# Kernel optimization log

Hardware: AMD Instinct MI355X
Metric: run time of the kernel (lower is better)

## Reference

```python
import math
import jax, jax.numpy as jnp
import numpy as np

N_HEADS = 16  # matches init_kwargs n_heads

def setup_inputs() -> dict:
    key = jax.random.key(0)
    ks = jax.random.split(key, 6)
    B, T, D = 1, 2048, 1024
    x = jax.random.normal(ks[0], (B, T, D), dtype=jnp.float32)
    # binary causal mask, broadcast over batch: [B, T, T]
    mask = jnp.broadcast_to(jnp.tril(jnp.ones((T, T), dtype=jnp.float32)), (B, T, T))
    shift = jax.random.uniform(ks[1], (B, T, T), dtype=jnp.float32)
    W = jax.random.normal(ks[2], (D, 3 * D), dtype=jnp.float32) * (1.0 / math.sqrt(D))
    b = jnp.zeros((3 * D,), dtype=jnp.float32)
    Wo = jax.random.normal(ks[3], (D, D), dtype=jnp.float32) * (1.0 / math.sqrt(D))
    bo = jnp.zeros((D,), dtype=jnp.float32)
    return {"x": x, "mask": mask, "shift": shift, "W": W, "b": b, "Wo": Wo, "bo": bo}

def reference(x, mask, shift, W, b, Wo, bo):
    B, T, D = x.shape
    H = N_HEADS
    dh = D // H
    qkv = x @ W + b  # [B,T,3D]
    # torch: chunk(H) -> stack -> chunk(3): head h uses block [h*3*dh : (h+1)*3*dh],
    # split as (q, k, v) of size dh each => reshape last dim to (H, 3, dh)
    qkv = qkv.reshape(B, T, H, 3, dh)
    q = jnp.moveaxis(qkv[..., 0, :], 2, 0)  # [H,B,T,dh]
    k = jnp.moveaxis(qkv[..., 1, :], 2, 0)
    v = jnp.moveaxis(qkv[..., 2, :], 2, 0)
    logits = jnp.einsum('hbqd,hbkd->hbqk', q, k) / math.sqrt(dh)  # [H,B,T,T]
    logits = logits * mask - 1e6 * (1.0 - mask)  # mask [B,T,T] broadcasts over H
    # per-head ALiBi-like scale: exp(-log(2) * h / 2)
    scale = jnp.exp(-math.log(2.0) * jnp.arange(H, dtype=jnp.float32) / 2.0)
    logits = logits - scale.reshape(H, 1, 1, 1) * shift
    att = jax.nn.softmax(logits, axis=-1)
    o = jnp.einsum('hbqk,hbkd->hbqd', att, v)  # [H,B,T,dh]
    o = jnp.moveaxis(o, 0, 2).reshape(B, T, D)  # concat heads on last dim
    o = o @ Wo + bo
    k_out = jnp.moveaxis(k, 0, 2).reshape(B, T, D)
    v_out = jnp.moveaxis(v, 0, 2).reshape(B, T, D)
    return (o, k_out, v_out)
```

## Files before the change

kernel.cpp:

```cpp
#include <hip/hip_runtime.h>
#include <hip/hip_bf16.h>

typedef __attribute__((ext_vector_type(8))) short bfrag8;
typedef __attribute__((ext_vector_type(4))) short short4v;
typedef __attribute__((ext_vector_type(4))) float f32x4;
typedef __attribute__((ext_vector_type(8))) unsigned short ushort8;
typedef __attribute__((ext_vector_type(4))) unsigned short ushort4v;

__device__ __forceinline__ float bf2f(unsigned short u) {
  unsigned int v = ((unsigned int)u) << 16;
  return __builtin_bit_cast(float, v);
}
__device__ __forceinline__ unsigned short f2bf(float f) {
  unsigned int u = __builtin_bit_cast(unsigned int, f);
  u += 0x7fffu + ((u >> 16) & 1u);
  return (unsigned short)(u >> 16);
}

#define GLDS(gp, lp) __builtin_amdgcn_global_load_lds( \
    (__attribute__((address_space(1))) void*)(gp), \
    (__attribute__((address_space(3))) void*)(lp), 16, 0, 0)

__device__ __forceinline__ bool inputs_are_f32(const unsigned int* mw) {
  return mw[0] == 0x3F800000u;
}

__global__ __launch_bounds__(256) void prep_kernel(
    const void* __restrict__ x, const void* __restrict__ b,
    const void* __restrict__ bo, const void* __restrict__ W,
    const void* __restrict__ Wo,
    unsigned short* __restrict__ xc, unsigned short* __restrict__ bc,
    unsigned short* __restrict__ boc, unsigned short* __restrict__ Wt,
    unsigned short* __restrict__ Wot,
    const unsigned int* __restrict__ mw) {
  const bool isf32 = inputs_are_f32(mw);
  const int bid = blockIdx.x, tid = threadIdx.x;
  __shared__ unsigned short tile[64][72];

  if (bid < 2052) {
    const void* src; unsigned short* dst; int base, n4;
    if (bid < 2048)      { src = x;  dst = xc;  base = bid;        n4 = 2048 * 1024 / 4; }
    else if (bid < 2051) { src = b;  dst = bc;  base = bid - 2048; n4 = 3072 / 4; }
    else                 { src = bo; dst = boc; base = 0;          n4 = 1024 / 4; }
    int i = base * 256 + tid;
    if (i >= n4) return;
    ushort4v o;
    if (isf32) {
      const float* s = (const float*)src;
      o[0] = f2bf(s[i * 4 + 0]); o[1] = f2bf(s[i * 4 + 1]);
      o[2] = f2bf(s[i * 4 + 2]); o[3] = f2bf(s[i * 4 + 3]);
    } else {
      o = *(const ushort4v*)((const unsigned short*)src + (size_t)i * 4);
    }
    *(ushort4v*)(dst + (size_t)i * 4) = o;
    return;
  }

  const void* src; unsigned short* dst; int R, C, bx, by;
  if (bid < 2820) { src = W;  dst = Wt;  R = 1024; C = 3072;
                    int e = bid - 2052; bx = e % 48; by = e / 48; }
  else            { src = Wo; dst = Wot; R = 1024; C = 1024;
                    int e = bid - 2820; bx = e % 16; by = e / 16; }
  const int r0 = by << 6, c0 = bx << 6;
  #pragma unroll
  for (int i = 0; i < 16; ++i) {
    int e = i * 256 + tid;
    int r = e >> 6, c = e & 63;
    size_t idx = (size_t)(r0 + r) * C + c0 + c;
    tile[r][c] = isf32 ? f2bf(((const float*)src)[idx])
                       : ((const unsigned short*)src)[idx];
  }
  __syncthreads();
  #pragma unroll
  for (int i = 0; i < 16; ++i) {
    int e = i * 256 + tid;
    int c = e >> 6, r = e & 63;
    dst[(size_t)(c0 + c) * R + r0 + r] = tile[r][c];
  }
}

template <int BN, int EPI>
__global__ __launch_bounds__(256) void gemm_bt(
    const unsigned short* __restrict__ A,
    const unsigned short* __restrict__ Bt,
    const unsigned short* __restrict__ bias,
    unsigned short* __restrict__ Cbf,
    float* __restrict__ kout,
    float* __restrict__ vout,
    float* __restrict__ Cf,
    int M, int N, int K) {
  constexpr int NT = BN / 32;
  __shared__ __align__(16) unsigned short As[128 * 32];
  __shared__ __align__(16) unsigned short Bs[BN * 32];
  const int tid = threadIdx.x;
  const int wave = tid >> 6, lane = tid & 63;
  const int q8 = lane >> 4, l15 = lane & 15;
  const int m0 = blockIdx.y << 7, n0 = blockIdx.x * BN;
  const int wm = (wave >> 1) << 6, wn = (wave & 1) * (BN / 2);

  f32x4 acc[4][NT];
  #pragma unroll
  for (int i = 0; i < 4; ++i)
    #pragma unroll
    for (int t = 0; t < NT; ++t) acc[i][t] = (f32x4){0.f, 0.f, 0.f, 0.f};

  const int cidb = wave * 64 + lane;
  for (int k0 = 0; k0 < K; k0 += 32) {
    __syncthreads();
    #pragma unroll
    for (int j = 0; j < 2; ++j) {
      int cid = j * 256 + cidb;
      int row = cid >> 2, co = (cid & 3) << 3;
      GLDS(A + (size_t)(m0 + row) * K + k0 + co, As + (size_t)(j * 256 + wave * 64) * 8);
    }
    #pragma unroll
    for (int j = 0; j < BN / 64; ++j) {
      int cid = j * 256 + cidb;
      int row = cid >> 2, co = (cid & 3) << 3;
      GLDS(Bt + (size_t)(n0 + row) * K + k0 + co, Bs + (size_t)(j * 256 + wave * 64) * 8);
    }
    __builtin_amdgcn_s_waitcnt(0);
    __syncthreads();
    bfrag8 af[4], bfr[NT];
    #pragma unroll
    for (int i = 0; i < 4; ++i)
      af[i] = *(const bfrag8*)(As + (wm + i * 16 + l15) * 32 + q8 * 8);
    #pragma unroll
    for (int t = 0; t < NT; ++t)
      bfr[t] = *(const bfrag8*)(Bs + (wn + t * 16 + l15) * 32 + q8 * 8);
    #pragma unroll
    for (int i = 0; i < 4; ++i)
      #pragma unroll
      for (int t = 0; t < NT; ++t)
        acc[i][t] = __builtin_amdgcn_mfma_f32_16x16x32_bf16(af[i], bfr[t], acc[i][t], 0, 0, 0);
  }

  #pragma unroll
  for (int t = 0; t < NT; ++t) {
    const int col = n0 + wn + t * 16 + l15;
    const float bv = bf2f(bias[col]);
    #pragma unroll
    for (int i = 0; i < 4; ++i) {
      #pragma unroll
      for (int r = 0; r < 4; ++r) {
        const int row = m0 + wm + i * 16 + q8 * 4 + r;
        const float fv = acc[i][t][r] + bv;
        if (EPI) {
          Cbf[(size_t)row * N + col] = f2bf(fv);
          int h = col / 192, rr = col - h * 192;
          if (rr >= 128)      vout[(size_t)row * 1024 + h * 64 + (rr - 128)] = fv;
          else if (rr >= 64)  kout[(size_t)row * 1024 + h * 64 + (rr - 64)] = fv;
        } else {
          Cf[(size_t)row * N + col] = fv;
        }
      }
    }
  }
}

__global__ __launch_bounds__(256) void attn_kernel(
    const unsigned short* __restrict__ qkv,
    const void* __restrict__ shift,
    unsigned short* __restrict__ Pon,
    float* __restrict__ Mst,
    float* __restrict__ Lst,
    const unsigned int* __restrict__ mw) {
  const bool isf32 = inputs_are_f32(mw);
  __shared__ __align__(16) unsigned short Qs[64 * 64];
  __shared__ __align__(16) unsigned short Ks[64 * 64];
  __shared__ __align__(16) unsigned short VTs[64 * 64];
  __shared__ __align__(16) short Ps[4 * 16 * 64];

  const int tid = threadIdx.x;
  const int wave = tid >> 6, lane = tid & 63;
  const int q8 = lane >> 4, l15 = lane & 15;
  const int bid = blockIdx.x;
  const int qb = 31 - (bid >> 5);
  const int h = bid & 15, part = (bid >> 4) & 1;
  const int q0 = qb << 6;
  const int count = qb + 1, c0 = (count + 1) >> 1;
  const int kbeg = part ? c0 : 0;
  const int kend = part ? count : c0;
  const float scale_h = exp2f(-0.5f * (float)h);
  const float NEG = -1e30f;

  #pragma unroll
  for (int j = 0; j < 2; ++j) {
    int cid = j * 256 + wave * 64 + lane;
    int row = cid >> 3, ci = cid & 7;
    ushort8 qv = *(const ushort8*)(qkv + (size_t)(q0 + row) * 3072 + h * 192 + ci * 8);
    *(ushort8*)(Qs + row * 64 + ((ci ^ (row & 7)) << 3)) = qv;
  }

  const int cidA = wave * 64 + lane;
  const int rowA = cidA >> 3, ciA = cidA & 7;
  const int cidB = 256 + cidA;
  const int rowB = cidB >> 3, ciB = cidB & 7;

  float mrow = NEG, lrow = 0.f;
  f32x4 oacc[4];
  #pragma unroll
  for (int t = 0; t < 4; ++t) oacc[t] = (f32x4){0.f, 0.f, 0.f, 0.f};
  const int qg = q0 + wave * 16 + l15;

  ushort8 kpfA, kpfB, vpf0, vpf1;
  float shf_nxt[4][4], shf_cur[4][4];

  {
    const int k0 = kbeg << 6;
    kpfA = *(const ushort8*)(qkv + (size_t)(k0 + rowA) * 3072 + h * 192 + 64 + ciA * 8);
    kpfB = *(const ushort8*)(qkv + (size_t)(k0 + rowB) * 3072 + h * 192 + 64 + ciB * 8);
    const unsigned short* vsrc = qkv + (size_t)(k0 + lane) * 3072 + h * 192 + 128 + wave * 16;
    vpf0 = *(const ushort8*)(vsrc);
    vpf1 = *(const ushort8*)(vsrc + 8);
    if (isf32) {
      const float* sp = (const float*)shift + (size_t)qg * 2048 + k0 + q8 * 4;
      #pragma unroll
      for (int mt = 0; mt < 4; ++mt) {
        f32x4 t4 = *(const f32x4*)(sp + mt * 16);
        shf_nxt[mt][0] = t4[0]; shf_nxt[mt][1] = t4[1];
        shf_nxt[mt][2] = t4[2]; shf_nxt[mt][3] = t4[3];
      }
    } else {
      const unsigned short* sp = (const unsigned short*)shift + (size_t)qg * 2048 + k0 + q8 * 4;
      #pragma unroll
      for (int mt = 0; mt < 4; ++mt) {
        ushort4v t4 = *(const ushort4v*)(sp + mt * 16);
        shf_nxt[mt][0] = bf2f(t4[0]); shf_nxt[mt][1] = bf2f(t4[1]);
        shf_nxt[mt][2] = bf2f(t4[2]); shf_nxt[mt][3] = bf2f(t4[3]);
      }
    }
  }

  for (int kt = kbeg; kt < kend; ++kt) {
    const int k0 = kt << 6;
    __syncthreads();
    *(ushort8*)(Ks + rowA * 64 + ((ciA ^ (rowA & 7)) << 3)) = kpfA;
    *(ushort8*)(Ks + rowB * 64 + ((ciB ^ (rowB & 7)) << 3)) = kpfB;
    #pragma unroll
    for (int j = 0; j < 8; ++j) {
      int d = wave * 16 + j;
      VTs[d * 64 + (((lane >> 3) ^ (d & 7)) << 3) + (lane & 7)] = vpf0[j];
      int d2 = d + 8;
      VTs[d2 * 64 + (((lane >> 3) ^ (d2 & 7)) << 3) + (lane & 7)] = vpf1[j];
    }
    #pragma unroll
    for (int mt = 0; mt < 4; ++mt)
      #pragma unroll
      for (int r = 0; r < 4; ++r) shf_cur[mt][r] = shf_nxt[mt][r];
    __syncthreads();

    if (kt + 1 < kend) {
      const int k0n = k0 + 64;
      kpfA = *(const ushort8*)(qkv + (size_t)(k0n + rowA) * 3072 + h * 192 + 64 + ciA * 8);
      kpfB = *(const ushort8*)(qkv + (size_t)(k0n + rowB) * 3072 + h * 192 + 64 + ciB * 8);
      const unsigned short* vsrc = qkv + (size_t)(k0n + lane) * 3072 + h * 192 + 128 + wave * 16;
      vpf0 = *(const ushort8*)(vsrc);
      vpf1 = *(const ushort8*)(vsrc + 8);
      if (isf32) {
        const float* sp = (const float*)shift + (size_t)qg * 2048 + k0n + q8 * 4;
        #pragma unroll
        for (int mt = 0; mt < 4; ++mt) {
          f32x4 t4 = *(const f32x4*)(sp + mt * 16);
          shf_nxt[mt][0] = t4[0]; shf_nxt[mt][1] = t4[1];
          shf_nxt[mt][2] = t4[2]; shf_nxt[mt][3] = t4[3];
        }
      } else {
        const unsigned short* sp = (const unsigned short*)shift + (size_t)qg * 2048 + k0n + q8 * 4;
        #pragma unroll
        for (int mt = 0; mt < 4; ++mt) {
          ushort4v t4 = *(const ushort4v*)(sp + mt * 16);
          shf_nxt[mt][0] = bf2f(t4[0]); shf_nxt[mt][1] = bf2f(t4[1]);
          shf_nxt[mt][2] = bf2f(t4[2]); shf_nxt[mt][3] = bf2f(t4[3]);
        }
      }
    }

    f32x4 st[4];
    #pragma unroll
    for (int mt = 0; mt < 4; ++mt) st[mt] = (f32x4){0.f, 0.f, 0.f, 0.f};
    #pragma unroll
    for (int kk = 0; kk < 2; ++kk) {
      int kc = kk * 4 + q8;
      int qrow = wave * 16 + l15;
      bfrag8 bq = *(const bfrag8*)(Qs + qrow * 64 + ((kc ^ (qrow & 7)) << 3));
      #pragma unroll
      for (int mt = 0; mt < 4; ++mt) {
        int krow = mt * 16 + l15;
        bfrag8 ak = *(const bfrag8*)(Ks + krow * 64 + ((kc ^ (krow & 7)) << 3));
        st[mt] = __builtin_amdgcn_mfma_f32_16x16x32_bf16(ak, bq, st[mt], 0, 0, 0);
      }
    }

    const bool diag = (kt == qb);
    float sv[4][4];
    float tmax = NEG;
    #pragma unroll
    for (int mt = 0; mt < 4; ++mt)
      #pragma unroll
      for (int r = 0; r < 4; ++r) {
        float s = st[mt][r] * 0.125f - scale_h * shf_cur[mt][r];
        if (diag) {
          int kg = k0 + mt * 16 + q8 * 4 + r;
          if (kg > qg) s = NEG;
        }
        sv[mt][r] = s;
        tmax = fmaxf(tmax, s);
      }
    tmax = fmaxf(tmax, __shfl_xor(tmax, 16, 64));
    tmax = fmaxf(tmax, __shfl_xor(tmax, 32, 64));
    const float mnew = fmaxf(mrow, tmax);
    const float alpha = __expf(mrow - mnew);
    float psum = 0.f;
    #pragma unroll
    for (int mt = 0; mt < 4; ++mt)
      #pragma unroll
      for (int r = 0; r < 4; ++r) {
        float p = __expf(sv[mt][r] - mnew);
        sv[mt][r] = p;
        psum += p;
      }
    psum += __shfl_xor(psum, 16, 64);
    psum += __shfl_xor(psum, 32, 64);
    lrow = lrow * alpha + psum;
    mrow = mnew;

    short* pw = Ps + wave * 1024;
    #pragma unroll
    for (int mt = 0; mt < 4; ++mt) {
      short4v pk;
      pk[0] = (short)f2bf(sv[mt][0]); pk[1] = (short)f2bf(sv[mt][1]);
      pk[2] = (short)f2bf(sv[mt][2]); pk[3] = (short)f2bf(sv[mt][3]);
      int kb = mt * 16 + q8 * 4;
      int chunk = (kb >> 3) ^ (l15 & 7);
      *(short4v*)(pw + l15 * 64 + (chunk << 3) + (kb & 7)) = pk;
    }

    float oal[4];
    #pragma unroll
    for (int r = 0; r < 4; ++r)
      oal[r] = __shfl(alpha, (lane & 48) | (q8 * 4 + r), 64);
    #pragma unroll
    for (int t = 0; t < 4; ++t)
      #pragma unroll
      for (int r = 0; r < 4; ++r) oacc[t][r] *= oal[r];

    __builtin_amdgcn_s_waitcnt(0xc07f);

    #pragma unroll
    for (int kk = 0; kk < 2; ++kk) {
      int kc = kk * 4 + q8;
      bfrag8 ap = *(const bfrag8*)(pw + l15 * 64 + ((kc ^ (l15 & 7)) << 3));
      #pragma unroll
      for (int t = 0; t < 4; ++t) {
        int drow = t * 16 + l15;
        bfrag8 bv = *(const bfrag8*)(VTs + drow * 64 + ((kc ^ (drow & 7)) << 3));
        oacc[t] = __builtin_amdgcn_mfma_f32_16x16x32_bf16(ap, bv, oacc[t], 0, 0, 0);
      }
    }
  }

  float linv[4];
  #pragma unroll
  for (int r = 0; r < 4; ++r) {
    float lr = __shfl(lrow, (lane & 48) | (q8 * 4 + r), 64);
    linv[r] = lr > 0.f ? 1.f / lr : 0.f;
  }
  const size_t pbase = ((size_t)(part * 16 + h) * 32 + qb) * 4096;
  #pragma unroll
  for (int t = 0; t < 4; ++t)
    #pragma unroll
    for (int r = 0; r < 4; ++r) {
      int rowl = wave * 16 + q8 * 4 + r;
      int coll = t * 16 + l15;
      Pon[pbase + rowl * 64 + coll] = f2bf(oacc[t][r] * linv[r]);
    }
  if (q8 == 0) {
    const size_t sbase = ((size_t)(part * 16 + h) * 32 + qb) * 64 + wave * 16 + l15;
    Mst[sbase] = mrow;
    Lst[sbase] = lrow;
  }
}

__global__ __launch_bounds__(256) void attn_merge(
    const unsigned short* __restrict__ Pon,
    const float* __restrict__ Mst, const float* __restrict__ Lst,
    unsigned short* __restrict__ oheads) {
  const int bid = blockIdx.x;
  const int h = bid >> 5, qb = bid & 31;
  const int t = threadIdx.x;
  const int q = t >> 2, dp = (t & 3) << 4;
  const size_t b0 = ((size_t)(0 * 16 + h) * 32 + qb);
  const size_t b1 = ((size_t)(1 * 16 + h) * 32 + qb);
  const float m0 = Mst[b0 * 64 + q], m1 = Mst[b1 * 64 + q];
  const float l0 = Lst[b0 * 64 + q], l1 = Lst[b1 * 64 + q];
  const float m = fmaxf(m0, m1);
  const float w0 = __expf(m0 - m) * l0, w1 = __expf(m1 - m) * l1;
  const float inv = 1.f / (w0 + w1);
  const unsigned short* p0 = Pon + b0 * 4096 + q * 64 + dp;
  const unsigned short* p1 = Pon + b1 * 4096 + q * 64 + dp;
  ushort8 a0 = *(const ushort8*)p0;
  ushort8 a1 = *(const ushort8*)(p0 + 8);
  ushort8 c0v = *(const ushort8*)p1;
  ushort8 c1v = *(const ushort8*)(p1 + 8);
  unsigned short* dst = oheads + (size_t)(qb * 64 + q) * 1024 + h * 64 + dp;
  ushort8 o0, o1;
  #pragma unroll
  for (int j = 0; j < 8; ++j) {
    o0[j] = f2bf((w0 * bf2f(a0[j]) + w1 * bf2f(c0v[j])) * inv);
    o1[j] = f2bf((w0 * bf2f(a1[j]) + w1 * bf2f(c1v[j])) * inv);
  }
  *(ushort8*)dst = o0;
  *(ushort8*)(dst + 8) = o1;
}

extern "C" void kernel_launch(void* const* d_in, const int* in_sizes, int n_in,
                              void* d_out, int out_size, void* d_ws, size_t ws_size,
                              hipStream_t stream) {
  const void* x     = d_in[0];
  const unsigned int* maskw = (const unsigned int*)d_in[1];
  const void* shift = d_in[2];
  const void* W     = d_in[3];
  const void* b     = d_in[4];
  const void* Wo    = d_in[5];
  const void* bo    = d_in[6];

  float* out   = (float*)d_out;
  float* o_out = out;
  float* k_out = out + (size_t)2048 * 1024;
  float* v_out = out + (size_t)2 * 2048 * 1024;

  unsigned short* ws     = (unsigned short*)d_ws;
  unsigned short* xc     = ws;
  unsigned short* bc     = xc + (size_t)2048 * 1024;
  unsigned short* boc    = bc + 3072;
  unsigned short* qkv    = boc + 1024;
  unsigned short* Wt     = qkv + (size_t)2048 * 3072;
  unsigned short* Wot    = Wt + (size_t)3072 * 1024;
  unsigned short* oheads = Wot + (size_t)1024 * 1024;
  unsigned short* Pon    = oheads + (size_t)2048 * 1024;
  float*          Mst    = (float*)(Pon + (size_t)2 * 16 * 32 * 4096);
  float*          Lst    = Mst + 65536;

  prep_kernel<<<3076, 256, 0, stream>>>(x, b, bo, W, Wo,
                                        xc, bc, boc, Wt, Wot, maskw);

  gemm_bt<128, 1><<<dim3(24, 16), 256, 0, stream>>>(
      xc, Wt, bc, qkv, k_out, v_out, nullptr, 2048, 3072, 1024);

  attn_kernel<<<1024, 256, 0, stream>>>(qkv, shift, Pon, Mst, Lst, maskw);

  attn_merge<<<512, 256, 0, stream>>>(Pon, Mst, Lst, oheads);

  gemm_bt<64, 0><<<dim3(16, 16), 256, 0, stream>>>(
      oheads, Wot, boc, nullptr, nullptr, nullptr, o_out, 2048, 1024, 1024);
}
```

Before: 202.7 us.

## Split attention into fixed 8-tile KV chunks with exp2 softmax and lazy rescale

Attention work is now split into KV chunks of at most 8 tiles per query block (up to 4 parts), replacing the two-way split, and the merge kernel combines up to four partials. The goal is better load balance across the causal triangle and more blocks. It also folds the softmax scale into log2 space so exp2 can be used, skips the output rescale when the running max grows by no more than 8, packs bf16 with a hardware convert instruction, raises MFMA wave priority, and adds an occupancy hint to the launch bounds. The lazy rescale lets unnormalised values grow by up to 2^8, which bf16 P can still represent, though it costs some precision. The extra partials add merge traffic.

```diff
diff --git a/kernel.cpp b/kernel.cpp
--- a/kernel.cpp
+++ b/kernel.cpp
@@ -6,6 +6,7 @@
 typedef __attribute__((ext_vector_type(4))) float f32x4;
 typedef __attribute__((ext_vector_type(8))) unsigned short ushort8;
 typedef __attribute__((ext_vector_type(4))) unsigned short ushort4v;
+typedef __attribute__((ext_vector_type(2))) unsigned int uint2v;
 
 __device__ __forceinline__ float bf2f(unsigned short u) {
   unsigned int v = ((unsigned int)u) << 16;
@@ -15,6 +16,11 @@
   unsigned int u = __builtin_bit_cast(unsigned int, f);
   u += 0x7fffu + ((u >> 16) & 1u);
   return (unsigned short)(u >> 16);
+}
+__device__ __forceinline__ unsigned int cvtpk_bf16(float a, float b) {
+  unsigned int r;
+  asm("v_cvt_pk_bf16_f32 %0, %1, %2" : "=v"(r) : "v"(a), "v"(b));
+  return r;
 }
 
 #define GLDS(gp, lp) __builtin_amdgcn_global_load_lds( \
@@ -158,7 +164,7 @@
   }
 }
 
-__global__ __launch_bounds__(256) void attn_kernel(
+__global__ __launch_bounds__(256, 5) void attn_kernel(
     const unsigned short* __restrict__ qkv,
     const void* __restrict__ shift,
     unsigned short* __restrict__ Pon,
@@ -175,13 +181,18 @@
   const int wave = tid >> 6, lane = tid & 63;
   const int q8 = lane >> 4, l15 = lane & 15;
   const int bid = blockIdx.x;
-  const int qb = 31 - (bid >> 5);
-  const int h = bid & 15, part = (bid >> 4) & 1;
+  const int h = bid & 15;
+  int pi = bid >> 4;
+  int qb = 31;
+  for (;;) { int npp = 1 + (qb >> 3); if (pi < npp) break; pi -= npp; --qb; }
+  const int part = pi;
   const int q0 = qb << 6;
-  const int count = qb + 1, c0 = (count + 1) >> 1;
-  const int kbeg = part ? c0 : 0;
-  const int kend = part ? count : c0;
-  const float scale_h = exp2f(-0.5f * (float)h);
+  const int count = qb + 1;
+  const int kbeg = part << 3;
+  const int kend = (kbeg + 8 < count) ? (kbeg + 8) : count;
+  const float LOG2E = 1.4426950408889634f;
+  const float c1 = 0.125f * LOG2E;
+  const float scale2 = __builtin_amdgcn_exp2f(-0.5f * (float)h) * LOG2E;
   const float NEG = -1e30f;
 
   #pragma unroll
@@ -218,16 +229,16 @@
       #pragma unroll
       for (int mt = 0; mt < 4; ++mt) {
         f32x4 t4 = *(const f32x4*)(sp + mt * 16);
-        shf_nxt[mt][0] = t4[0]; shf_nxt[mt][1] = t4[1];
-        shf_nxt[mt][2] = t4[2]; shf_nxt[mt][3] = t4[3];
+        shf_nxt[mt][0] = scale2 * t4[0]; shf_nxt[mt][1] = scale2 * t4[1];
+        shf_nxt[mt][2] = scale2 * t4[2]; shf_nxt[mt][3] = scale2 * t4[3];
       }
     } else {
       const unsigned short* sp = (const unsigned short*)shift + (size_t)qg * 2048 + k0 + q8 * 4;
       #pragma unroll
       for (int mt = 0; mt < 4; ++mt) {
         ushort4v t4 = *(const ushort4v*)(sp + mt * 16);
-        shf_nxt[mt][0] = bf2f(t4[0]); shf_nxt[mt][1] = bf2f(t4[1]);
-        shf_nxt[mt][2] = bf2f(t4[2]); shf_nxt[mt][3] = bf2f(t4[3]);
+        shf_nxt[mt][0] = scale2 * bf2f(t4[0]); shf_nxt[mt][1] = scale2 * bf2f(t4[1]);
+        shf_nxt[mt][2] = scale2 * bf2f(t4[2]); shf_nxt[mt][3] = scale2 * bf2f(t4[3]);
       }
     }
   }
@@ -262,16 +273,16 @@
         #pragma unroll
         for (int mt = 0; mt < 4; ++mt) {
           f32x4 t4 = *(const f32x4*)(sp + mt * 16);
-          shf_nxt[mt][0] = t4[0]; shf_nxt[mt][1] = t4[1];
-          shf_nxt[mt][2] = t4[2]; shf_nxt[mt][3] = t4[3];
+          shf_nxt[mt][0] = scale2 * t4[0]; shf_nxt[mt][1] = scale2 * t4[1];
+          shf_nxt[mt][2] = scale2 * t4[2]; shf_nxt[mt][3] = scale2 * t4[3];
         }
       } else {
         const unsigned short* sp = (const unsigned short*)shift + (size_t)qg * 2048 + k0n + q8 * 4;
         #pragma unroll
         for (int mt = 0; mt < 4; ++mt) {
           ushort4v t4 = *(const ushort4v*)(sp + mt * 16);
-          shf_nxt[mt][0] = bf2f(t4[0]); shf_nxt[mt][1] = bf2f(t4[1]);
-          shf_nxt[mt][2] = bf2f(t4[2]); shf_nxt[mt][3] = bf2f(t4[3]);
+          shf_nxt[mt][0] = scale2 * bf2f(t4[0]); shf_nxt[mt][1] = scale2 * bf2f(t4[1]);
+          shf_nxt[mt][2] = scale2 * bf2f(t4[2]); shf_nxt[mt][3] = scale2 * bf2f(t4[3]);
         }
       }
     }
@@ -279,6 +290,7 @@
     f32x4 st[4];
     #pragma unroll
     for (int mt = 0; mt < 4; ++mt) st[mt] = (f32x4){0.f, 0.f, 0.f, 0.f};
+    __builtin_amdgcn_s_setprio(1);
     #pragma unroll
     for (int kk = 0; kk < 2; ++kk) {
       int kc = kk * 4 + q8;
@@ -291,6 +303,7 @@
         st[mt] = __builtin_amdgcn_mfma_f32_16x16x32_bf16(ak, bq, st[mt], 0, 0, 0);
       }
     }
+    __builtin_amdgcn_s_setprio(0);
 
     const bool diag = (kt == qb);
     float sv[4][4];
@@ -299,7 +312,7 @@
     for (int mt = 0; mt < 4; ++mt)
       #pragma unroll
       for (int r = 0; r < 4; ++r) {
-        float s = st[mt][r] * 0.125f - scale_h * shf_cur[mt][r];
+        float s = st[mt][r] * c1 - shf_cur[mt][r];
         if (diag) {
           int kg = k0 + mt * 16 + q8 * 4 + r;
           if (kg > qg) s = NEG;
@@ -309,44 +322,51 @@
       }
     tmax = fmaxf(tmax, __shfl_xor(tmax, 16, 64));
     tmax = fmaxf(tmax, __shfl_xor(tmax, 32, 64));
-    const float mnew = fmaxf(mrow, tmax);
-    const float alpha = __expf(mrow - mnew);
+    const int skip = __all(tmax - mrow <= 8.0f);
+    const float mnew = skip ? mrow : fmaxf(mrow, tmax);
     float psum = 0.f;
     #pragma unroll
     for (int mt = 0; mt < 4; ++mt)
       #pragma unroll
       for (int r = 0; r < 4; ++r) {
-        float p = __expf(sv[mt][r] - mnew);
+        float p = __builtin_amdgcn_exp2f(sv[mt][r] - mnew);
         sv[mt][r] = p;
         psum += p;
       }
     psum += __shfl_xor(psum, 16, 64);
     psum += __shfl_xor(psum, 32, 64);
-    lrow = lrow * alpha + psum;
-    mrow = mnew;
 
     short* pw = Ps + wave * 1024;
     #pragma unroll
     for (int mt = 0; mt < 4; ++mt) {
-      short4v pk;
-      pk[0] = (short)f2bf(sv[mt][0]); pk[1] = (short)f2bf(sv[mt][1]);
-      pk[2] = (short)f2bf(sv[mt][2]); pk[3] = (short)f2bf(sv[mt][3]);
+      unsigned int w0 = cvtpk_bf16(sv[mt][0], sv[mt][1]);
+      unsigned int w1 = cvtpk_bf16(sv[mt][2], sv[mt][3]);
+      uint2v u2; u2[0] = w0; u2[1] = w1;
+      short4v pk = __builtin_bit_cast(short4v, u2);
       int kb = mt * 16 + q8 * 4;
       int chunk = (kb >> 3) ^ (l15 & 7);
       *(short4v*)(pw + l15 * 64 + (chunk << 3) + (kb & 7)) = pk;
     }
 
-    float oal[4];
-    #pragma unroll
-    for (int r = 0; r < 4; ++r)
-      oal[r] = __shfl(alpha, (lane & 48) | (q8 * 4 + r), 64);
-    #pragma unroll
-    for (int t = 0; t < 4; ++t)
-      #pragma unroll
-      for (int r = 0; r < 4; ++r) oacc[t][r] *= oal[r];
+    if (skip) {
+      lrow += psum;
+    } else {
+      const float alpha = __builtin_amdgcn_exp2f(mrow - mnew);
+      lrow = lrow * alpha + psum;
+      mrow = mnew;
+      float oal[4];
+      #pragma unroll
+      for (int r = 0; r < 4; ++r)
+        oal[r] = __shfl(alpha, (lane & 48) | (q8 * 4 + r), 64);
+      #pragma unroll
+      for (int t = 0; t < 4; ++t)
+        #pragma unroll
+        for (int r = 0; r < 4; ++r) oacc[t][r] *= oal[r];
+    }
 
     __builtin_amdgcn_s_waitcnt(0xc07f);
 
+    __builtin_amdgcn_s_setprio(1);
     #pragma unroll
     for (int kk = 0; kk < 2; ++kk) {
       int kc = kk * 4 + q8;
@@ -358,6 +378,7 @@
         oacc[t] = __builtin_amdgcn_mfma_f32_16x16x32_bf16(ap, bv, oacc[t], 0, 0, 0);
       }
     }
+    __builtin_amdgcn_s_setprio(0);
   }
 
   float linv[4];
@@ -366,7 +387,8 @@
     float lr = __shfl(lrow, (lane & 48) | (q8 * 4 + r), 64);
     linv[r] = lr > 0.f ? 1.f / lr : 0.f;
   }
-  const size_t pbase = ((size_t)(part * 16 + h) * 32 + qb) * 4096;
+  const size_t slot = (size_t)(h * 32 + qb) * 4 + part;
+  const size_t pbase = slot * 4096;
   #pragma unroll
   for (int t = 0; t < 4; ++t)
     #pragma unroll
@@ -376,7 +398,7 @@
       Pon[pbase + rowl * 64 + coll] = f2bf(oacc[t][r] * linv[r]);
     }
   if (q8 == 0) {
-    const size_t sbase = ((size_t)(part * 16 + h) * 32 + qb) * 64 + wave * 16 + l15;
+    const size_t sbase = slot * 64 + wave * 16 + l15;
     Mst[sbase] = mrow;
     Lst[sbase] = lrow;
   }
@@ -388,27 +410,47 @@
     unsigned short* __restrict__ oheads) {
   const int bid = blockIdx.x;
   const int h = bid >> 5, qb = bid & 31;
+  const int np = 1 + (qb >> 3);
   const int t = threadIdx.x;
   const int q = t >> 2, dp = (t & 3) << 4;
-  const size_t b0 = ((size_t)(0 * 16 + h) * 32 + qb);
-  const size_t b1 = ((size_t)(1 * 16 + h) * 32 + qb);
-  const float m0 = Mst[b0 * 64 + q], m1 = Mst[b1 * 64 + q];
-  const float l0 = Lst[b0 * 64 + q], l1 = Lst[b1 * 64 + q];
-  const float m = fmaxf(m0, m1);
-  const float w0 = __expf(m0 - m) * l0, w1 = __expf(m1 - m) * l1;
-  const float inv = 1.f / (w0 + w1);
-  const unsigned short* p0 = Pon + b0 * 4096 + q * 64 + dp;
-  const unsigned short* p1 = Pon + b1 * 4096 + q * 64 + dp;
-  ushort8 a0 = *(const ushort8*)p0;
-  ushort8 a1 = *(const ushort8*)(p0 + 8);
-  ushort8 c0v = *(const ushort8*)p1;
-  ushort8 c1v = *(const ushort8*)(p1 + 8);
+  const size_t slot0 = (size_t)(h * 32 + qb) * 4;
+  float mv[4], lv[4];
+  float m = -1e30f;
+  #pragma unroll
+  for (int p = 0; p < 4; ++p) {
+    mv[p] = (p < np) ? Mst[(slot0 + p) * 64 + q] : -1e30f;
+    lv[p] = (p < np) ? Lst[(slot0 + p) * 64 + q] : 0.f;
+    m = fmaxf(m, mv[p]);
+  }
+  float w[4], wsum = 0.f;
+  #pragma unroll
+  for (int p = 0; p < 4; ++p) {
+    w[p] = __builtin_amdgcn_exp2f(mv[p] - m) * lv[p];
+    wsum += w[p];
+  }
+  const float inv = 1.f / wsum;
+  float acc0[8], acc1[8];
+  #pragma unroll
+  for (int j = 0; j < 8; ++j) { acc0[j] = 0.f; acc1[j] = 0.f; }
+  #pragma unroll
+  for (int p = 0; p < 4; ++p) {
+    if (p < np) {
+      const unsigned short* pp = Pon + (slot0 + p) * 4096 + q * 64 + dp;
+      ushort8 a0 = *(const ushort8*)pp;
+      ushort8 a1 = *(const ushort8*)(pp + 8);
+      #pragma unroll
+      for (int j = 0; j < 8; ++j) {
+        acc0[j] += w[p] * bf2f(a0[j]);
+        acc1[j] += w[p] * bf2f(a1[j]);
+      }
+    }
+  }
   unsigned short* dst = oheads + (size_t)(qb * 64 + q) * 1024 + h * 64 + dp;
   ushort8 o0, o1;
   #pragma unroll
   for (int j = 0; j < 8; ++j) {
-    o0[j] = f2bf((w0 * bf2f(a0[j]) + w1 * bf2f(c0v[j])) * inv);
-    o1[j] = f2bf((w0 * bf2f(a1[j]) + w1 * bf2f(c1v[j])) * inv);
+    o0[j] = f2bf(acc0[j] * inv);
+    o1[j] = f2bf(acc1[j] * inv);
   }
   *(ushort8*)dst = o0;
   *(ushort8*)(dst + 8) = o1;
@@ -439,8 +481,8 @@
   unsigned short* Wot    = Wt + (size_t)3072 * 1024;
   unsigned short* oheads = Wot + (size_t)1024 * 1024;
   unsigned short* Pon    = oheads + (size_t)2048 * 1024;
-  float*          Mst    = (float*)(Pon + (size_t)2 * 16 * 32 * 4096);
-  float*          Lst    = Mst + 65536;
+  float*          Mst    = (float*)(Pon + (size_t)16 * 32 * 4 * 4096);
+  float*          Lst    = Mst + 131072;
 
   prep_kernel<<<3076, 256, 0, stream>>>(x, b, bo, W, Wo,
                                         xc, bc, boc, Wt, Wot, maskw);
@@ -448,7 +490,7 @@
   gemm_bt<128, 1><<<dim3(24, 16), 256, 0, stream>>>(
       xc, Wt, bc, qkv, k_out, v_out, nullptr, 2048, 3072, 1024);
 
-  attn_kernel<<<1024, 256, 0, stream>>>(qkv, shift, Pon, Mst, Lst, maskw);
+  attn_kernel<<<1280, 256, 0, stream>>>(qkv, shift, Pon, Mst, Lst, maskw);
 
   attn_merge<<<512, 256, 0, stream>>>(Pon, Mst, Lst, oheads);
 
```

After: 289.5 us. 1.43x slower.
